# Performance work log

Hardware: AMD Instinct MI355X
Metric: run time of the kernel (lower is better)

The kernel has to match this reference:

```python
import jax, jax.numpy as jnp
from jax import lax
import numpy as np

B, C_IN, C_OUT, H, W = 16, 64, 64, 160, 160
K, STRIDE, PAD, DIL, SHIFT = 3, 1, 1, 1, 1


def setup_inputs() -> dict:
    key = jax.random.key(0)
    kx, kw = jax.random.split(key)
    x = jax.random.normal(kx, (B, C_IN, H, W), dtype=jnp.float32)
    weight = jax.random.normal(kw, (C_OUT, C_IN, K, K), dtype=jnp.float32)
    return {"x": x, "weight": weight}


def reference(x, weight):
    Bn, C, Hh, Ww = x.shape
    # zero-pad spatially by shift_distance on all sides (matches F.pad)
    xp = jnp.pad(x, ((0, 0), (0, 0), (SHIFT, SHIFT), (SHIFT, SHIFT)))
    Hp, Wp = Hh + 2 * SHIFT, Ww + 2 * SHIFT
    # shifts list: (dx, dy) for channel groups c % 5
    dxs = jnp.array([0, SHIFT, 0, -SHIFT, 0])
    dys = jnp.array([0, 0, SHIFT, 0, -SHIFT])
    cmod = jnp.arange(C) % 5
    dy = dys[cmod]  # [C] roll along H (dim 2)
    dx = dxs[cmod]  # [C] roll along W (dim 3)
    # torch.roll semantics: out[h, w] = in[(h - dy) % Hp, (w - dx) % Wp]
    row = (jnp.arange(Hp)[None, :] - dy[:, None]) % Hp  # [C, Hp]
    col = (jnp.arange(Wp)[None, :] - dx[:, None]) % Wp  # [C, Wp]
    # single fused gather over channel-dependent row/col indices
    x_shifted = xp[:, jnp.arange(C)[:, None, None], row[:, :, None], col[:, None, :]]
    out = lax.conv_general_dilated(
        x_shifted, weight,
        window_strides=(STRIDE, STRIDE),
        padding=((PAD, PAD), (PAD, PAD)),
        rhs_dilation=(DIL, DIL),
        dimension_numbers=("NCHW", "OIHW", "NCHW"),
    )
    # crop the extra border introduced by the pre-pad
    return out[:, :, 1:-1, 1:-1]
```

## Files before the change

kernel.cpp:

```cpp
#include <hip/hip_runtime.h>
#include <hip/hip_bf16.h>

#define BATCH 16
#define CIN 64
#define COUT 64
#define HH 160
#define WW 160
#define HP 162
#define WP 162

#define ABUF 21760
#define PSTR 161

typedef __attribute__((ext_vector_type(8))) __bf16 bf16x8;
typedef __attribute__((ext_vector_type(4))) float f32x4;
typedef __attribute__((ext_vector_type(8))) unsigned short ushort8;

typedef __attribute__((address_space(1))) const unsigned int gu32;
typedef __attribute__((address_space(3))) unsigned int lu32;

__global__ __launch_bounds__(256) void prep(const float* __restrict__ x,
                                            const float* __restrict__ w,
                                            unsigned short* __restrict__ xs,
                                            unsigned short* __restrict__ wb) {
  __shared__ float lds[64 * PSTR];

  if (blockIdx.x >= BATCH * HP) {
    int e = (blockIdx.x - BATCH * HP) * 256 + threadIdx.x;
    if (e < 9 * 64 * 64) {
      int tap = e >> 12;
      int o = (e >> 6) & 63;
      int c = e & 63;
      float v = w[((size_t)(o * 64 + c)) * 9 + tap];
      __hip_bfloat16 h = __float2bfloat16(v);
      wb[e] = *reinterpret_cast<unsigned short*>(&h);
    }
    return;
  }

  int y = blockIdx.x % HP;
  int b = blockIdx.x / HP;
  int tid = threadIdx.x;

#pragma unroll
  for (int it = 0; it < 10; ++it) {
    int idx = it * 256 + tid;
    int c = idx / 40;
    int j = idx - c * 40;
    int cm = c % 5;
    int dy = (cm == 2) ? 1 : ((cm == 4) ? -1 : 0);
    int yy = y - dy;
    f32x4 v = {0.f, 0.f, 0.f, 0.f};
    if (yy >= 1 && yy <= HH)
      v = *reinterpret_cast<const f32x4*>(
          x + (((size_t)(b * CIN + c)) * HH + (size_t)(yy - 1)) * WW + j * 4);
    int p0 = c * PSTR + 4 * j;
#pragma unroll
    for (int e = 0; e < 4; ++e) lds[p0 + e] = v[e];
  }
  __syncthreads();

  int cg = tid & 7;
  int xr = tid >> 3;
  int dxe[8], rowb[8];
#pragma unroll
  for (int e = 0; e < 8; ++e) {
    int c = cg * 8 + e;
    int cm = c % 5;
    dxe[e] = (cm == 1) ? 1 : ((cm == 3) ? -1 : 0);
    rowb[e] = c * PSTR;
  }
  size_t obase = ((size_t)(b * HP + y) * WP) * CIN + cg * 8;
#pragma unroll
  for (int it = 0; it < 6; ++it) {
    int xi = it * 32 + xr;
    if (xi < WP) {
      ushort8 val;
#pragma unroll
      for (int e = 0; e < 8; ++e) {
        int xx = xi - dxe[e] - 1;
        float v = 0.f;
        if (xx >= 0 && xx < WW) v = lds[rowb[e] + xx];
        __hip_bfloat16 h = __float2bfloat16(v);
        val[e] = *reinterpret_cast<unsigned short*>(&h);
      }
      *reinterpret_cast<ushort8*>(xs + obase + (size_t)xi * CIN) = val;
    }
  }
}

__global__ __launch_bounds__(1024, 4) void conv_mfma(const unsigned short* __restrict__ xs,
                                                     const unsigned short* __restrict__ wb,
                                                     float* __restrict__ out) {
  __shared__ __align__(16) unsigned short lds_a[ABUF];
  __shared__ __align__(16) unsigned short lds_b[ABUF];
  __shared__ __align__(16) unsigned short lds_w[9 * 64 * 64];

  int tid = threadIdx.x;
  int blk = blockIdx.x;
  int tile0 = (blk & 7) * 32 + (blk >> 3);
  int ntiles = (tile0 < 64) ? 7 : 6;

  int wv = tid >> 6;
  int rw = wv >> 1;
  int nh = wv & 1;
  int lane = tid & 63;
  int l15 = lane & 15;
  int q = lane >> 4;

  int goff[3];
#pragma unroll
  for (int r = 0; r < 3; ++r) {
    int u = r * 1024 + tid;
    int p = u >> 3;
    int j = (u & 7) ^ (p & 7);
    int pr = p / 34, pc = p - pr * 34;
    goff[r] = (pr * WP + pc) * CIN + j * 8;
  }

  int bw0 = l15 * 64 + ((q ^ (l15 & 7)) * 8);
  int bw1 = l15 * 64 + (((4 + q) ^ (l15 & 7)) * 8);

#define STAGE_TO(BUFARR, T_)                                                   \
  {                                                                            \
    int sb_ = (T_) / 100;                                                      \
    int srr_ = (T_) - sb_ * 100;                                               \
    int sti_ = srr_ / 5, stj_ = srr_ - sti_ * 5;                               \
    const unsigned short* srcb_ = xs +                                         \
        ((size_t)sb_ * HP + (size_t)(sti_ * 8)) * WP * CIN +                   \
        (size_t)(stj_ * 32) * CIN;                                             \
    _Pragma("unroll") for (int r = 0; r < 3; ++r) {                            \
      int u_ = r * 1024 + tid;                                                 \
      if (u_ < 2720)                                                           \
        __builtin_amdgcn_global_load_lds((gu32*)(srcb_ + goff[r]),             \
                                         (lu32*)((BUFARR) + (u_ & ~63) * 8),   \
                                         16, 0, 0);                            \
    }                                                                          \
  }

#define LOAD_A(RBUF, bufp, tt)                                                 \
  {                                                                            \
    const int ch_ = (tt) / 9, ky_ = ((tt) % 9) / 3, kx_ = (tt) % 3;            \
    _Pragma("unroll") for (int mt = 0; mt < 2; ++mt) {                         \
      int pix = (rw + ky_) * 34 + kx_ + l15 + mt * 16;                         \
      int chunk = (ch_ * 4 + q) ^ (pix & 7);                                   \
      Ab[bufp][mt] =                                                           \
          *reinterpret_cast<const bf16x8*>(&(RBUF)[pix * 64 + chunk * 8]);     \
    }                                                                          \
  }

#define LOAD_BW(bufp, tt)                                                      \
  {                                                                            \
    const int ch_ = (tt) / 9, tap_ = (tt) % 9;                                 \
    _Pragma("unroll") for (int ns = 0; ns < 2; ++ns)                           \
        Bb[bufp][ns] = *reinterpret_cast<const bf16x8*>(                       \
            &lds_w[tap_ * 4096 + (nh * 2 + ns) * 1024 + (ch_ ? bw1 : bw0)]);   \
  }

#define TILE_BODY(I_, RBUF, WBUF)                                              \
  {                                                                            \
    int t_ = tile0 + 256 * (I_);                                               \
    int b_ = t_ / 100;                                                         \
    int rr_ = t_ - b_ * 100;                                                   \
    int ti_ = rr_ / 5, tj_ = rr_ - ti_ * 5;                                    \
    int y0_ = ti_ * 8, x0_ = tj_ * 32;                                         \
    if ((I_) + 1 < ntiles) STAGE_TO(WBUF, tile0 + 256 * ((I_) + 1));           \
    _Pragma("unroll") for (int a_ = 0; a_ < 2; ++a_)                           \
      _Pragma("unroll") for (int c2_ = 0; c2_ < 2; ++c2_)                      \
        acc[a_][c2_] = (f32x4){0.f, 0.f, 0.f, 0.f};                            \
    LOAD_A(RBUF, 0, 0);                                                        \
    LOAD_BW(0, 0);                                                             \
    _Pragma("unroll") for (int tt = 0; tt < 18; ++tt) {                        \
      if (tt + 1 < 18) {                                                       \
        LOAD_A(RBUF, (tt + 1) & 1, tt + 1);                                    \
        LOAD_BW((tt + 1) & 1, tt + 1);                                         \
      }                                                                        \
      __builtin_amdgcn_s_setprio(1);                                           \
      _Pragma("unroll") for (int mt = 0; mt < 2; ++mt)                         \
        _Pragma("unroll") for (int ns = 0; ns < 2; ++ns)                       \
          acc[mt][ns] = __builtin_amdgcn_mfma_f32_16x16x32_bf16(               \
              Ab[tt & 1][mt], Bb[tt & 1][ns], acc[mt][ns], 0, 0, 0);           \
      __builtin_amdgcn_s_setprio(0);                                           \
    }                                                                          \
    __syncthreads();                                                           \
    _Pragma("unroll") for (int mt = 0; mt < 2; ++mt) {                         \
      int orow_ = y0_ + rw;                                                    \
      int xo_ = x0_ + mt * 16 + q * 4;                                         \
      _Pragma("unroll") for (int ns = 0; ns < 2; ++ns) {                       \
        int o_ = nh * 32 + ns * 16 + l15;                                      \
        *reinterpret_cast<f32x4*>(                                             \
            out + ((size_t)(b_ * COUT + o_) * HH + (size_t)orow_) * WW + xo_) = \
            acc[mt][ns];                                                       \
      }                                                                        \
    }                                                                          \
  }

  f32x4 acc[2][2];
  bf16x8 Ab[2][2];
  bf16x8 Bb[2][2];

#pragma unroll
  for (int r = 0; r < 5; ++r) {
    int u = r * 1024 + tid;
    if (u < 4608) {
      int orow = u >> 3;
      int jj = (u & 7) ^ (orow & 7);
      __builtin_amdgcn_global_load_lds((gu32*)(wb + orow * 64 + jj * 8),
                                       (lu32*)(lds_w + (u & ~63) * 8), 16, 0, 0);
    }
  }
  STAGE_TO(lds_a, tile0);
  __syncthreads();

  for (int i = 0; i < ntiles; i += 2) {
    TILE_BODY(i, lds_a, lds_b);
    if (i + 1 < ntiles) TILE_BODY(i + 1, lds_b, lds_a);
  }

#undef TILE_BODY
#undef LOAD_BW
#undef LOAD_A
#undef STAGE_TO
}

extern "C" void kernel_launch(void* const* d_in, const int* in_sizes, int n_in,
                              void* d_out, int out_size, void* d_ws, size_t ws_size,
                              hipStream_t stream) {
  const float* x = (const float*)d_in[0];
  const float* w = (const float*)d_in[1];
  float* out = (float*)d_out;

  unsigned short* xs = (unsigned short*)d_ws;
  unsigned short* wb = (unsigned short*)((char*)d_ws + (size_t)BATCH * HP * WP * CIN * 2);

  hipLaunchKernelGGL(prep, dim3(BATCH * HP + 144), dim3(256), 0, stream, x, w, xs, wb);
  hipLaunchKernelGGL(conv_mfma, dim3(256), dim3(1024), 0, stream, xs, wb, out);
}
```

Before: 226.2 us.

## Switch conv to 32x32x16 MFMA tiles and contiguous per-block tile ranges

Each wave now computes a 32-pixel by 32-output-channel tile with four 32x32x16 bf16 MFMAs per tap, replacing four 16x16x32 MFMAs per half-channel step. This halves the unrolled loop trips and changes the LDS fragment loads and the output write pattern. Blocks now take contiguous tile ranges rather than a strided interleave, which changes L2 locality for the staged input. The larger accumulator raises register pressure, and the new LDS read patterns could bring bank conflicts.

Result: slower. 272.3 us (+20.4%).

```diff
diff --git a/kernel.cpp b/kernel.cpp
--- a/kernel.cpp
+++ b/kernel.cpp
@@ -14,6 +14,7 @@
 
 typedef __attribute__((ext_vector_type(8))) __bf16 bf16x8;
 typedef __attribute__((ext_vector_type(4))) float f32x4;
+typedef __attribute__((ext_vector_type(16))) float f32x16;
 typedef __attribute__((ext_vector_type(8))) unsigned short ushort8;
 
 typedef __attribute__((address_space(1))) const unsigned int gu32;
@@ -98,15 +99,19 @@
 
   int tid = threadIdx.x;
   int blk = blockIdx.x;
-  int tile0 = (blk & 7) * 32 + (blk >> 3);
-  int ntiles = (tile0 < 64) ? 7 : 6;
+  int start = blk * 6 + (blk < 64 ? blk : 64);
+  int ntiles = 6 + (blk < 64 ? 1 : 0);
 
   int wv = tid >> 6;
   int rw = wv >> 1;
-  int nh = wv & 1;
+  int og = wv & 1;
   int lane = tid & 63;
-  int l15 = lane & 15;
-  int q = lane >> 4;
+  int m31 = lane & 31;
+  int q2 = lane >> 5;
+  int l7 = lane & 7;
+
+  int pbase = rw * 34 + m31;
+  int bwl = (og * 32 + m31) * 64;
 
   int goff[3];
 #pragma unroll
@@ -117,9 +122,6 @@
     int pr = p / 34, pc = p - pr * 34;
     goff[r] = (pr * WP + pc) * CIN + j * 8;
   }
-
-  int bw0 = l15 * 64 + ((q ^ (l15 & 7)) * 8);
-  int bw1 = l15 * 64 + (((4 + q) ^ (l15 & 7)) * 8);
 
 #define STAGE_TO(BUFARR, T_)                                                   \
   {                                                                            \
@@ -138,66 +140,54 @@
     }                                                                          \
   }
 
-#define LOAD_A(RBUF, bufp, tt)                                                 \
+#define LOAD_AB(RBUF, bufp, tt)                                                \
   {                                                                            \
-    const int ch_ = (tt) / 9, ky_ = ((tt) % 9) / 3, kx_ = (tt) % 3;            \
-    _Pragma("unroll") for (int mt = 0; mt < 2; ++mt) {                         \
-      int pix = (rw + ky_) * 34 + kx_ + l15 + mt * 16;                         \
-      int chunk = (ch_ * 4 + q) ^ (pix & 7);                                   \
-      Ab[bufp][mt] =                                                           \
-          *reinterpret_cast<const bf16x8*>(&(RBUF)[pix * 64 + chunk * 8]);     \
-    }                                                                          \
-  }
-
-#define LOAD_BW(bufp, tt)                                                      \
-  {                                                                            \
-    const int ch_ = (tt) / 9, tap_ = (tt) % 9;                                 \
-    _Pragma("unroll") for (int ns = 0; ns < 2; ++ns)                           \
-        Bb[bufp][ns] = *reinterpret_cast<const bf16x8*>(                       \
-            &lds_w[tap_ * 4096 + (nh * 2 + ns) * 1024 + (ch_ ? bw1 : bw0)]);   \
+    const int ky_ = (tt) / 3, kx_ = (tt) % 3;                                  \
+    int pix_ = pbase + ky_ * 34 + kx_;                                         \
+    int px7_ = pix_ & 7;                                                       \
+    _Pragma("unroll") for (int ks = 0; ks < 4; ++ks) {                         \
+      int ca_ = (ks * 2 + q2) ^ px7_;                                          \
+      Ab[bufp][ks] = *reinterpret_cast<const bf16x8*>(                         \
+          &(RBUF)[pix_ * 64 + ca_ * 8]);                                       \
+      int cb_ = (ks * 2 + q2) ^ l7;                                            \
+      Bb[bufp][ks] = *reinterpret_cast<const bf16x8*>(                         \
+          &lds_w[(tt) * 4096 + bwl + cb_ * 8]);                                \
+    }                                                                          \
   }
 
 #define TILE_BODY(I_, RBUF, WBUF)                                              \
   {                                                                            \
-    int t_ = tile0 + 256 * (I_);                                               \
+    int t_ = start + (I_);                                                     \
     int b_ = t_ / 100;                                                         \
     int rr_ = t_ - b_ * 100;                                                   \
     int ti_ = rr_ / 5, tj_ = rr_ - ti_ * 5;                                    \
     int y0_ = ti_ * 8, x0_ = tj_ * 32;                                         \
-    if ((I_) + 1 < ntiles) STAGE_TO(WBUF, tile0 + 256 * ((I_) + 1));           \
-    _Pragma("unroll") for (int a_ = 0; a_ < 2; ++a_)                           \
-      _Pragma("unroll") for (int c2_ = 0; c2_ < 2; ++c2_)                      \
-        acc[a_][c2_] = (f32x4){0.f, 0.f, 0.f, 0.f};                            \
-    LOAD_A(RBUF, 0, 0);                                                        \
-    LOAD_BW(0, 0);                                                             \
-    _Pragma("unroll") for (int tt = 0; tt < 18; ++tt) {                        \
-      if (tt + 1 < 18) {                                                       \
-        LOAD_A(RBUF, (tt + 1) & 1, tt + 1);                                    \
-        LOAD_BW((tt + 1) & 1, tt + 1);                                         \
-      }                                                                        \
+    if ((I_) + 1 < ntiles) STAGE_TO(WBUF, start + (I_) + 1);                   \
+    _Pragma("unroll") for (int e_ = 0; e_ < 16; ++e_) acc[e_] = 0.f;           \
+    LOAD_AB(RBUF, 0, 0);                                                       \
+    _Pragma("unroll") for (int tt = 0; tt < 9; ++tt) {                         \
+      if (tt + 1 < 9) LOAD_AB(RBUF, (tt + 1) & 1, tt + 1);                     \
       __builtin_amdgcn_s_setprio(1);                                           \
-      _Pragma("unroll") for (int mt = 0; mt < 2; ++mt)                         \
-        _Pragma("unroll") for (int ns = 0; ns < 2; ++ns)                       \
-          acc[mt][ns] = __builtin_amdgcn_mfma_f32_16x16x32_bf16(               \
-              Ab[tt & 1][mt], Bb[tt & 1][ns], acc[mt][ns], 0, 0, 0);           \
+      _Pragma("unroll") for (int ks = 0; ks < 4; ++ks)                         \
+          acc = __builtin_amdgcn_mfma_f32_32x32x16_bf16(                       \
+              Ab[tt & 1][ks], Bb[tt & 1][ks], acc, 0, 0, 0);                   \
       __builtin_amdgcn_s_setprio(0);                                           \
     }                                                                          \
     __syncthreads();                                                           \
-    _Pragma("unroll") for (int mt = 0; mt < 2; ++mt) {                         \
-      int orow_ = y0_ + rw;                                                    \
-      int xo_ = x0_ + mt * 16 + q * 4;                                         \
-      _Pragma("unroll") for (int ns = 0; ns < 2; ++ns) {                       \
-        int o_ = nh * 32 + ns * 16 + l15;                                      \
-        *reinterpret_cast<f32x4*>(                                             \
-            out + ((size_t)(b_ * COUT + o_) * HH + (size_t)orow_) * WW + xo_) = \
-            acc[mt][ns];                                                       \
-      }                                                                        \
-    }                                                                          \
-  }
-
-  f32x4 acc[2][2];
-  bf16x8 Ab[2][2];
-  bf16x8 Bb[2][2];
+    int orow_ = y0_ + rw;                                                      \
+    int obch_ = og * 32 + m31;                                                 \
+    _Pragma("unroll") for (int g = 0; g < 4; ++g) {                            \
+      f32x4 v_ = {acc[4 * g], acc[4 * g + 1], acc[4 * g + 2], acc[4 * g + 3]}; \
+      int xo_ = x0_ + g * 8 + q2 * 4;                                          \
+      *reinterpret_cast<f32x4*>(                                               \
+          out + ((size_t)(b_ * COUT + obch_) * HH + (size_t)orow_) * WW +      \
+          xo_) = v_;                                                           \
+    }                                                                          \
+  }
+
+  f32x16 acc;
+  bf16x8 Ab[2][4];
+  bf16x8 Bb[2][4];
 
 #pragma unroll
   for (int r = 0; r < 5; ++r) {
@@ -209,7 +199,7 @@
                                        (lu32*)(lds_w + (u & ~63) * 8), 16, 0, 0);
     }
   }
-  STAGE_TO(lds_a, tile0);
+  STAGE_TO(lds_a, start);
   __syncthreads();
 
   for (int i = 0; i < ntiles; i += 2) {
@@ -218,8 +208,7 @@
   }
 
 #undef TILE_BODY
-#undef LOAD_BW
-#undef LOAD_A
+#undef LOAD_AB
 #undef STAGE_TO
 }
 
```
